# Performance work log

Measured on AMD Instinct MI355X. Metric: run time of the kernel, lower is better.

## Reference

```python
import jax, jax.numpy as jnp
import numpy as np

NLAYERS = 4
HEADS = 4
HEAD_DIM = 64
C = HEADS * HEAD_DIM  # 256
MAX_LEN = 1024


def setup_inputs() -> dict:
    key = jax.random.key(0)
    k1, k2, k3 = jax.random.split(key, 3)
    B, S = 16, 1024
    x = jax.random.normal(k1, (B, C, 1, S), dtype=jnp.float32)
    # length is only used via its static shape[0]; values are irrelevant
    length = jnp.zeros((MAX_LEN,), dtype=jnp.int32)
    # per-layer 1x1 conv weights, std=0.1 as in the torch init (squeeze the 1x1 spatial dims)
    w = jax.random.normal(k2, (NLAYERS, C, C), dtype=jnp.float32) * 0.1
    # persistent kv buffer
    kv = jax.random.normal(k3, (NLAYERS, HEADS, MAX_LEN, HEAD_DIM), dtype=jnp.float32) * 0.1
    return {"x": x, "length": length, "w": w, "kv": kv}


def reference(x, length, w, kv):
    B, _, _, S = x.shape
    L = length.shape[0]  # static slice length into kv buffer
    scale = 1.0 / jnp.sqrt(jnp.asarray(HEAD_DIM, dtype=x.dtype))
    for i in range(NLAYERS):
        # 1x1 conv == channel projection: (B,C,1,S) -> (B,C,1,S)
        x = jnp.einsum('oc,bchs->bohs', w[i], x)
        # view (B,4,64,S) then permute -> query (B,H,S,D)
        q = x.reshape(B, HEADS, HEAD_DIM, S).transpose(0, 1, 3, 2)
        kvi = kv[i, :, :L]  # (H, L, D); broadcasts over batch like the (1,H,L,D) torch slice
        # scaled dot-product attention with k == v == kvi
        scores = jnp.einsum('bhsd,hld->bhsl', q, kvi) * scale
        attn = jax.nn.softmax(scores, axis=-1)
        o = jnp.einsum('bhsl,hld->bhsd', attn, kvi)  # (B,H,S,D)
        # permute back and merge heads -> (B,256,1,S)
        x = o.transpose(0, 1, 3, 2).reshape(B, C, 1, S)
    return x
```

## Files before the change

kernel.cpp:

```cpp
#include <hip/hip_runtime.h>

#define NL   4
#define NH   4
#define HD   64
#define CD   256
#define SQL  1024
#define BB   16

typedef _Float16 half8 __attribute__((ext_vector_type(8)));
typedef _Float16 half4 __attribute__((ext_vector_type(4)));
typedef _Float16 half2v __attribute__((ext_vector_type(2)));
typedef float    f32x4 __attribute__((ext_vector_type(4)));
typedef float    f32x16 __attribute__((ext_vector_type(16)));
typedef unsigned short u16x8 __attribute__((ext_vector_type(8)));
typedef unsigned int  uint4v __attribute__((ext_vector_type(4)));

static __device__ __forceinline__ float bf2f(unsigned short u) {
    union { unsigned int i; float f; } v; v.i = ((unsigned int)u) << 16; return v.f;
}
static __device__ __forceinline__ unsigned short f2bf(float f) {
    union { float f; unsigned int i; } v; v.f = f;
    unsigned int u = v.i;
    return (unsigned short)((u + 0x7fffu + ((u >> 16) & 1u)) >> 16);
}

static __device__ __forceinline__ int detect_flag(const void* win) {
    const unsigned int* w = (const unsigned int*)win;
    int cnt = 0;
#pragma unroll 1
    for (int i = 0; i < 64; i++) {
        unsigned int lo = w[i] & 0xFFFFu;
        int e = (int)((lo >> 7) & 0xFF);
        cnt += (e >= 96 && e <= 144) ? 1 : 0;
    }
    return cnt >= 48 ? 1 : 0;
}

__global__ __launch_bounds__(256) void prep_all(const void* __restrict__ xin,
                                                const void* __restrict__ win,
                                                const void* __restrict__ kvin,
                                                _Float16* __restrict__ x16,
                                                _Float16* __restrict__ w16,
                                                _Float16* __restrict__ kaF,
                                                _Float16* __restrict__ vtF) {
    __shared__ __align__(16) _Float16 tile[64][72];
    const int bi = blockIdx.x;
    const int t = threadIdx.x;
    const int isbf = detect_flag(win);

    if (bi < 1024) {
        const int st = bi & 15, ct = (bi >> 4) & 3, b = bi >> 6;
        const int r = t >> 2, seg = t & 3;
        const size_t base = ((size_t)(b * CD + ct * 64 + r)) * SQL + st * 64 + seg * 16;
        float v[16];
        if (isbf) {
            const unsigned short* src = (const unsigned short*)xin + base;
            u16x8 u0 = *(const u16x8*)(src);
            u16x8 u1 = *(const u16x8*)(src + 8);
#pragma unroll
            for (int j = 0; j < 8; j++) { v[j] = bf2f(u0[j]); v[8 + j] = bf2f(u1[j]); }
        } else {
            const float* src = (const float*)xin + base;
#pragma unroll
            for (int c = 0; c < 4; c++) {
                f32x4 a = *(const f32x4*)(src + c * 4);
#pragma unroll
                for (int j = 0; j < 4; j++) v[c * 4 + j] = a[j];
            }
        }
#pragma unroll
        for (int j = 0; j < 16; j++) tile[r][seg * 16 + j] = (_Float16)v[j];
        __syncthreads();
        half8 o0, o1;
#pragma unroll
        for (int j = 0; j < 8; j++) { o0[j] = tile[seg * 16 + j][r]; o1[j] = tile[seg * 16 + 8 + j][r]; }
        _Float16* dt = x16 + ((size_t)(b * SQL + st * 64 + r)) * CD + ct * 64 + seg * 16;
        *(half8*)(dt) = o0;
        *(half8*)(dt + 8) = o1;
    } else if (bi < 1280) {
        const int j2 = bi - 1024;
        const int lt = j2 & 15, ih = j2 >> 4;
        const int r = t >> 2, seg = t & 3;
        const size_t base = ((size_t)(ih * SQL + lt * 64 + r)) * HD + seg * 16;
        float v[16];
        if (isbf) {
            const unsigned short* src = (const unsigned short*)kvin + base;
            u16x8 u0 = *(const u16x8*)(src);
            u16x8 u1 = *(const u16x8*)(src + 8);
#pragma unroll
            for (int j = 0; j < 8; j++) { v[j] = bf2f(u0[j]); v[8 + j] = bf2f(u1[j]); }
        } else {
            const float* src = (const float*)kvin + base;
#pragma unroll
            for (int c = 0; c < 4; c++) {
                f32x4 a = *(const f32x4*)(src + c * 4);
#pragma unroll
                for (int j = 0; j < 4; j++) v[c * 4 + j] = a[j];
            }
        }
#pragma unroll
        for (int j = 0; j < 16; j++) tile[r][seg * 16 + j] = (_Float16)v[j];
        __syncthreads();
        const int l = t & 63, hie = l >> 5, lne = l & 31;
        _Float16* kaB = kaF + ((size_t)ih << 16);
        _Float16* vtB = vtF + ((size_t)ih << 16);
#pragma unroll
        for (int it = 0; it < 2; it++) {
            const int c = (t >> 6) + it * 4;
            half8 ok = *(const half8*)(&tile[(c >> 2) * 32 + lne][(c & 3) * 16 + hie * 8]);
            half8 ov;
#pragma unroll
            for (int j = 0; j < 8; j++)
                ov[j] = tile[(c & 3) * 16 + hie * 8 + j][(c >> 2) * 32 + lne];
            *(half8*)(kaB + ((lt * 8 + c) << 9) + l * 8) = ok;
            *(half8*)(vtB + ((lt * 8 + c) << 9) + l * 8) = ov;
        }
    } else {
        const int i = (bi - 1280) * 256 + t;
        const size_t base = (size_t)i * 8;
        half8 h;
        if (isbf) {
            u16x8 u = *(const u16x8*)((const unsigned short*)win + base);
#pragma unroll
            for (int j = 0; j < 8; j++) h[j] = (_Float16)bf2f(u[j]);
        } else {
            const float* p = (const float*)win + base;
            f32x4 a0 = *(const f32x4*)(p);
            f32x4 a1 = *(const f32x4*)(p + 4);
#pragma unroll
            for (int j = 0; j < 4; j++) { h[j] = (_Float16)a0[j]; h[4 + j] = (_Float16)a1[j]; }
        }
        *(half8*)(w16 + base) = h;
    }
}

__global__ __launch_bounds__(256, 2) void layer_fused(const _Float16* __restrict__ xg,
                                                      _Float16* __restrict__ xout,
                                                      const _Float16* __restrict__ w16,
                                                      const _Float16* __restrict__ kaF,
                                                      const _Float16* __restrict__ vtF,
                                                      const void* __restrict__ win,
                                                      void* __restrict__ outp,
                                                      int L) {
    __shared__ __align__(16) _Float16 kvbuf[2][16384];
    const int sb = blockIdx.x;
    const int h  = blockIdx.y;
    const int b  = blockIdx.z;
    const int t  = threadIdx.x;
    const int wv = t >> 6, lane = t & 63, ln = lane & 31, hi = lane >> 5;
    const int s0 = sb * 128 + wv * 32;

    const _Float16* kaB = kaF + ((size_t)(L * NH + h) << 16);
    const _Float16* vtB = vtF + ((size_t)(L * NH + h) << 16);

    auto stage = [&](int lt, int buf, int hf) {
#pragma unroll
        for (int j = 0; j < 4; j++) {
            const int c = wv * 4 + j;
            const _Float16* src = (c < 8)
                ? kaB + (((lt * 8 + c) << 9))
                : vtB + (((lt * 8 + (c - 8)) << 9));
            __builtin_amdgcn_global_load_lds(
                (const __attribute__((address_space(1))) void*)(src + lane * 8),
                (__attribute__((address_space(3))) void*)(&kvbuf[buf][hf * 8192 + c * 512]),
                16, 0, 0);
        }
    };

    stage(0, 0, 0);
    stage(1, 0, 1);

    f32x16 gacc[2];
#pragma unroll
    for (int dblk = 0; dblk < 2; dblk++)
#pragma unroll
        for (int r = 0; r < 16; r++) gacc[dblk][r] = 0.0f;
    const _Float16* wb = w16 + ((size_t)L << 16) + ((size_t)(h * 64) << 8);
#pragma unroll
    for (int kc = 0; kc < 16; kc++) {
        half8 bx = *(const half8*)(xg + ((size_t)((b << 10) + s0 + ln) << 8) + kc * 16 + hi * 8);
#pragma unroll
        for (int dblk = 0; dblk < 2; dblk++) {
            half8 aw = *(const half8*)(wb + ((size_t)(dblk * 32 + ln) << 8) + kc * 16 + hi * 8);
            gacc[dblk] = __builtin_amdgcn_mfma_f32_32x32x16_f16(aw, bx, gacc[dblk], 0, 0, 0);
        }
    }

    const float sc = 0.180336880111120f;
    half8 qb[4];
#pragma unroll
    for (int dblk = 0; dblk < 2; dblk++)
#pragma unroll
        for (int k1 = 0; k1 < 2; k1++) {
            unsigned int u01 = __builtin_bit_cast(unsigned int,
                __builtin_amdgcn_cvt_pkrtz(gacc[dblk][k1 * 8 + 0] * sc, gacc[dblk][k1 * 8 + 1] * sc));
            unsigned int u23 = __builtin_bit_cast(unsigned int,
                __builtin_amdgcn_cvt_pkrtz(gacc[dblk][k1 * 8 + 2] * sc, gacc[dblk][k1 * 8 + 3] * sc));
            unsigned int w01 = __builtin_bit_cast(unsigned int,
                __builtin_amdgcn_cvt_pkrtz(gacc[dblk][k1 * 8 + 4] * sc, gacc[dblk][k1 * 8 + 5] * sc));
            unsigned int w23 = __builtin_bit_cast(unsigned int,
                __builtin_amdgcn_cvt_pkrtz(gacc[dblk][k1 * 8 + 6] * sc, gacc[dblk][k1 * 8 + 7] * sc));
            asm("v_permlane32_swap_b32 %0, %1" : "+v"(u01), "+v"(w01));
            asm("v_permlane32_swap_b32 %0, %1" : "+v"(u23), "+v"(w23));
            uint4v q; q[0] = u01; q[1] = u23; q[2] = w01; q[3] = w23;
            qb[dblk * 2 + k1] = __builtin_bit_cast(half8, q);
        }

    f32x16 oacc[2];
#pragma unroll
    for (int dblk = 0; dblk < 2; dblk++)
#pragma unroll
        for (int r = 0; r < 16; r++) oacc[dblk][r] = 0.0f;
    f32x4 rsum;
#pragma unroll
    for (int r = 0; r < 4; r++) rsum[r] = 0.0f;

    __syncthreads();

#pragma unroll 1
    for (int ltp = 0; ltp < 8; ltp++) {
        const int buf = ltp & 1;
        if (ltp < 7) { stage(2 * ltp + 2, buf ^ 1, 0); stage(2 * ltp + 3, buf ^ 1, 1); }
#pragma unroll
        for (int sub = 0; sub < 2; sub++) {
            const _Float16* base = &kvbuf[buf][sub * 8192];
            half8 kab[8];
#pragma unroll
            for (int c = 0; c < 8; c++)
                kab[c] = *(const half8*)(base + c * 512 + lane * 8);

            f32x16 stt[2];
#pragma unroll
            for (int lblk = 0; lblk < 2; lblk++)
#pragma unroll
                for (int r = 0; r < 16; r++) stt[lblk][r] = 0.0f;
            __builtin_amdgcn_s_setprio(1);
#pragma unroll
            for (int lblk = 0; lblk < 2; lblk++)
#pragma unroll
                for (int kd = 0; kd < 4; kd++)
                    stt[lblk] = __builtin_amdgcn_mfma_f32_32x32x16_f16(
                        kab[lblk * 4 + kd], qb[kd], stt[lblk], 0, 0, 0);
            __builtin_amdgcn_s_setprio(0);

            half8 vab[8];
#pragma unroll
            for (int c = 0; c < 8; c++)
                vab[c] = *(const half8*)(base + (8 + c) * 512 + lane * 8);

            half8 pb[4];
#pragma unroll
            for (int lblk = 0; lblk < 2; lblk++) {
                float e[16];
#pragma unroll
                for (int r = 0; r < 16; r++) e[r] = __builtin_amdgcn_exp2f(stt[lblk][r]);
#pragma unroll
                for (int g = 0; g < 4; g++)
                    rsum[g] += (e[g * 4 + 0] + e[g * 4 + 1]) + (e[g * 4 + 2] + e[g * 4 + 3]);
#pragma unroll
                for (int k1 = 0; k1 < 2; k1++) {
                    unsigned int u01 = __builtin_bit_cast(unsigned int,
                        __builtin_amdgcn_cvt_pkrtz(e[k1 * 8 + 0], e[k1 * 8 + 1]));
                    unsigned int u23 = __builtin_bit_cast(unsigned int,
                        __builtin_amdgcn_cvt_pkrtz(e[k1 * 8 + 2], e[k1 * 8 + 3]));
                    unsigned int w01 = __builtin_bit_cast(unsigned int,
                        __builtin_amdgcn_cvt_pkrtz(e[k1 * 8 + 4], e[k1 * 8 + 5]));
                    unsigned int w23 = __builtin_bit_cast(unsigned int,
                        __builtin_amdgcn_cvt_pkrtz(e[k1 * 8 + 6], e[k1 * 8 + 7]));
                    asm("v_permlane32_swap_b32 %0, %1" : "+v"(u01), "+v"(w01));
                    asm("v_permlane32_swap_b32 %0, %1" : "+v"(u23), "+v"(w23));
                    uint4v p; p[0] = u01; p[1] = u23; p[2] = w01; p[3] = w23;
                    pb[lblk * 2 + k1] = __builtin_bit_cast(half8, p);
                }
            }

            __builtin_amdgcn_s_setprio(1);
#pragma unroll
            for (int dblk = 0; dblk < 2; dblk++)
#pragma unroll
                for (int ks = 0; ks < 4; ks++)
                    oacc[dblk] = __builtin_amdgcn_mfma_f32_32x32x16_f16(
                        vab[dblk * 4 + ks], pb[ks], oacc[dblk], 0, 0, 0);
            __builtin_amdgcn_s_setprio(0);
        }
        __syncthreads();
    }

    float rs = (rsum[0] + rsum[1]) + (rsum[2] + rsum[3]);
    unsigned int ra = __builtin_bit_cast(unsigned int, rs);
    unsigned int rb = ra;
    asm("" : "+v"(rb));
    asm("v_permlane32_swap_b32 %0, %1" : "+v"(ra), "+v"(rb));
    const float inv = 1.0f / (__builtin_bit_cast(float, ra) + __builtin_bit_cast(float, rb));
    const int s = s0 + ln;

    if (L < NL - 1) {
#pragma unroll
        for (int dblk = 0; dblk < 2; dblk++)
#pragma unroll
            for (int q2 = 0; q2 < 4; q2++) {
                half4 hv;
#pragma unroll
                for (int r = 0; r < 4; r++) hv[r] = (_Float16)(oacc[dblk][q2 * 4 + r] * inv);
                *(half4*)(xout + (((size_t)((b << 10) + s)) << 8) +
                          (h << 6) + dblk * 32 + q2 * 8 + hi * 4) = hv;
            }
    } else if (detect_flag(win)) {
#pragma unroll
        for (int dblk = 0; dblk < 2; dblk++)
#pragma unroll
            for (int q2 = 0; q2 < 4; q2++)
#pragma unroll
                for (int r = 0; r < 4; r++) {
                    const int c = (h << 6) + dblk * 32 + q2 * 8 + hi * 4 + r;
                    ((unsigned short*)outp)[(((size_t)(b * CD + c)) << 10) + s] =
                        f2bf(oacc[dblk][q2 * 4 + r] * inv);
                }
    } else {
#pragma unroll
        for (int dblk = 0; dblk < 2; dblk++)
#pragma unroll
            for (int q2 = 0; q2 < 4; q2++)
#pragma unroll
                for (int r = 0; r < 4; r++) {
                    const int c = (h << 6) + dblk * 32 + q2 * 8 + hi * 4 + r;
                    ((float*)outp)[(((size_t)(b * CD + c)) << 10) + s] =
                        oacc[dblk][q2 * 4 + r] * inv;
                }
    }
}

extern "C" void kernel_launch(void* const* d_in, const int* in_sizes, int n_in,
                              void* d_out, int out_size, void* d_ws, size_t ws_size,
                              hipStream_t stream) {
    const void* xin = d_in[0];
    const void* win = d_in[2];
    const void* kvin = d_in[3];

    char* ws = (char*)d_ws;
    const size_t MB = 1u << 20;
    _Float16* xa  = (_Float16*)(ws);
    _Float16* xb  = (_Float16*)(ws + 8 * MB);
    _Float16* w16 = (_Float16*)(ws + 16 * MB);
    _Float16* kaF = (_Float16*)(ws + 17 * MB);
    _Float16* vtF = (_Float16*)(ws + 19 * MB);

    prep_all<<<dim3(1024 + 256 + 128), 256, 0, stream>>>(xin, win, kvin, xa, w16, kaF, vtF);

    _Float16* cur = xa;
    _Float16* nxt = xb;
    for (int i = 0; i < NL; i++) {
        layer_fused<<<dim3(SQL / 128, NH, BB), 256, 0, stream>>>(cur, nxt, w16, kaF, vtF,
                                                                 win, d_out, i);
        _Float16* tmp = cur; cur = nxt; nxt = tmp;
    }
}
```

Baseline: 204.4 us.

## Process two query sub-tiles per wave to reuse staged KV across more rows

Each wave now handles 64 query rows (two 32-row sub-tiles) instead of 32, so each K/V tile loaded into LDS and read into registers is reused for twice as many queries, and the grid is halved. Waves alternate which half of the staged KV buffer they process first, presumably to spread LDS bank traffic. The dtype detection flag is computed once in the prep kernel and passed through workspace instead of rescanning weights in the final layer. The cost is doubled accumulator register pressure, with launch bounds lowered to one block per SIMD, which cuts occupancy and latency hiding.

```diff
diff --git a/kernel.cpp b/kernel.cpp
--- a/kernel.cpp
+++ b/kernel.cpp
@@ -25,14 +25,19 @@
 }
 
 static __device__ __forceinline__ int detect_flag(const void* win) {
-    const unsigned int* w = (const unsigned int*)win;
+    const uint4v* w = (const uint4v*)win;
     int cnt = 0;
-#pragma unroll 1
-    for (int i = 0; i < 64; i++) {
-        unsigned int lo = w[i] & 0xFFFFu;
-        int e = (int)((lo >> 7) & 0xFF);
-        cnt += (e >= 96 && e <= 144) ? 1 : 0;
-    }
+    uint4v u[16];
+#pragma unroll
+    for (int i = 0; i < 16; i++) u[i] = w[i];
+#pragma unroll
+    for (int i = 0; i < 16; i++)
+#pragma unroll
+        for (int j = 0; j < 4; j++) {
+            unsigned int lo = u[i][j] & 0xFFFFu;
+            int e = (int)((lo >> 7) & 0xFF);
+            cnt += (e >= 96 && e <= 144) ? 1 : 0;
+        }
     return cnt >= 48 ? 1 : 0;
 }
 
@@ -42,7 +47,8 @@
                                                 _Float16* __restrict__ x16,
                                                 _Float16* __restrict__ w16,
                                                 _Float16* __restrict__ kaF,
-                                                _Float16* __restrict__ vtF) {
+                                                _Float16* __restrict__ vtF,
+                                                int* __restrict__ flagp) {
     __shared__ __align__(16) _Float16 tile[64][72];
     const int bi = blockIdx.x;
     const int t = threadIdx.x;
@@ -116,6 +122,7 @@
             *(half8*)(vtB + ((lt * 8 + c) << 9) + l * 8) = ov;
         }
     } else {
+        if (bi == 1280 && t == 0) *flagp = isbf;
         const int i = (bi - 1280) * 256 + t;
         const size_t base = (size_t)i * 8;
         half8 h;
@@ -134,12 +141,12 @@
     }
 }
 
-__global__ __launch_bounds__(256, 2) void layer_fused(const _Float16* __restrict__ xg,
+__global__ __launch_bounds__(256, 1) void layer_fused(const _Float16* __restrict__ xg,
                                                       _Float16* __restrict__ xout,
                                                       const _Float16* __restrict__ w16,
                                                       const _Float16* __restrict__ kaF,
                                                       const _Float16* __restrict__ vtF,
-                                                      const void* __restrict__ win,
+                                                      const int* __restrict__ flagp,
                                                       void* __restrict__ outp,
                                                       int L) {
     __shared__ __align__(16) _Float16 kvbuf[2][16384];
@@ -148,7 +155,10 @@
     const int b  = blockIdx.z;
     const int t  = threadIdx.x;
     const int wv = t >> 6, lane = t & 63, ln = lane & 31, hi = lane >> 5;
-    const int s0 = sb * 128 + wv * 32;
+    const int s0 = sb * 256 + wv * 64;
+    const int par = (sb ^ h ^ b ^ wv) & 1;
+
+    const int isbf_final = (L == NL - 1) ? *flagp : 0;
 
     const _Float16* kaB = kaF + ((size_t)(L * NH + h) << 16);
     const _Float16* vtB = vtF + ((size_t)(L * NH + h) << 16);
@@ -170,163 +180,184 @@
     stage(0, 0, 0);
     stage(1, 0, 1);
 
-    f32x16 gacc[2];
-#pragma unroll
-    for (int dblk = 0; dblk < 2; dblk++)
-#pragma unroll
-        for (int r = 0; r < 16; r++) gacc[dblk][r] = 0.0f;
+    f32x16 gacc[2][2];
+#pragma unroll
+    for (int ns = 0; ns < 2; ns++)
+#pragma unroll
+        for (int dblk = 0; dblk < 2; dblk++)
+#pragma unroll
+            for (int r = 0; r < 16; r++) gacc[ns][dblk][r] = 0.0f;
     const _Float16* wb = w16 + ((size_t)L << 16) + ((size_t)(h * 64) << 8);
 #pragma unroll
     for (int kc = 0; kc < 16; kc++) {
-        half8 bx = *(const half8*)(xg + ((size_t)((b << 10) + s0 + ln) << 8) + kc * 16 + hi * 8);
+        half8 bx0 = *(const half8*)(xg + ((size_t)((b << 10) + s0 + ln) << 8) + kc * 16 + hi * 8);
+        half8 bx1 = *(const half8*)(xg + ((size_t)((b << 10) + s0 + 32 + ln) << 8) + kc * 16 + hi * 8);
 #pragma unroll
         for (int dblk = 0; dblk < 2; dblk++) {
             half8 aw = *(const half8*)(wb + ((size_t)(dblk * 32 + ln) << 8) + kc * 16 + hi * 8);
-            gacc[dblk] = __builtin_amdgcn_mfma_f32_32x32x16_f16(aw, bx, gacc[dblk], 0, 0, 0);
+            gacc[0][dblk] = __builtin_amdgcn_mfma_f32_32x32x16_f16(aw, bx0, gacc[0][dblk], 0, 0, 0);
+            gacc[1][dblk] = __builtin_amdgcn_mfma_f32_32x32x16_f16(aw, bx1, gacc[1][dblk], 0, 0, 0);
         }
     }
 
     const float sc = 0.180336880111120f;
-    half8 qb[4];
-#pragma unroll
-    for (int dblk = 0; dblk < 2; dblk++)
-#pragma unroll
-        for (int k1 = 0; k1 < 2; k1++) {
-            unsigned int u01 = __builtin_bit_cast(unsigned int,
-                __builtin_amdgcn_cvt_pkrtz(gacc[dblk][k1 * 8 + 0] * sc, gacc[dblk][k1 * 8 + 1] * sc));
-            unsigned int u23 = __builtin_bit_cast(unsigned int,
-                __builtin_amdgcn_cvt_pkrtz(gacc[dblk][k1 * 8 + 2] * sc, gacc[dblk][k1 * 8 + 3] * sc));
-            unsigned int w01 = __builtin_bit_cast(unsigned int,
-                __builtin_amdgcn_cvt_pkrtz(gacc[dblk][k1 * 8 + 4] * sc, gacc[dblk][k1 * 8 + 5] * sc));
-            unsigned int w23 = __builtin_bit_cast(unsigned int,
-                __builtin_amdgcn_cvt_pkrtz(gacc[dblk][k1 * 8 + 6] * sc, gacc[dblk][k1 * 8 + 7] * sc));
-            asm("v_permlane32_swap_b32 %0, %1" : "+v"(u01), "+v"(w01));
-            asm("v_permlane32_swap_b32 %0, %1" : "+v"(u23), "+v"(w23));
-            uint4v q; q[0] = u01; q[1] = u23; q[2] = w01; q[3] = w23;
-            qb[dblk * 2 + k1] = __builtin_bit_cast(half8, q);
-        }
-
-    f32x16 oacc[2];
-#pragma unroll
-    for (int dblk = 0; dblk < 2; dblk++)
-#pragma unroll
-        for (int r = 0; r < 16; r++) oacc[dblk][r] = 0.0f;
-    f32x4 rsum;
-#pragma unroll
-    for (int r = 0; r < 4; r++) rsum[r] = 0.0f;
+    half8 qb[2][4];
+#pragma unroll
+    for (int ns = 0; ns < 2; ns++)
+#pragma unroll
+        for (int dblk = 0; dblk < 2; dblk++)
+#pragma unroll
+            for (int k1 = 0; k1 < 2; k1++) {
+                unsigned int u01 = __builtin_bit_cast(unsigned int,
+                    __builtin_amdgcn_cvt_pkrtz(gacc[ns][dblk][k1 * 8 + 0] * sc, gacc[ns][dblk][k1 * 8 + 1] * sc));
+                unsigned int u23 = __builtin_bit_cast(unsigned int,
+                    __builtin_amdgcn_cvt_pkrtz(gacc[ns][dblk][k1 * 8 + 2] * sc, gacc[ns][dblk][k1 * 8 + 3] * sc));
+                unsigned int w01 = __builtin_bit_cast(unsigned int,
+                    __builtin_amdgcn_cvt_pkrtz(gacc[ns][dblk][k1 * 8 + 4] * sc, gacc[ns][dblk][k1 * 8 + 5] * sc));
+                unsigned int w23 = __builtin_bit_cast(unsigned int,
+                    __builtin_amdgcn_cvt_pkrtz(gacc[ns][dblk][k1 * 8 + 6] * sc, gacc[ns][dblk][k1 * 8 + 7] * sc));
+                asm("v_permlane32_swap_b32 %0, %1" : "+v"(u01), "+v"(w01));
+                asm("v_permlane32_swap_b32 %0, %1" : "+v"(u23), "+v"(w23));
+                uint4v q; q[0] = u01; q[1] = u23; q[2] = w01; q[3] = w23;
+                qb[ns][dblk * 2 + k1] = __builtin_bit_cast(half8, q);
+            }
+
+    f32x16 oacc[2][2];
+#pragma unroll
+    for (int ns = 0; ns < 2; ns++)
+#pragma unroll
+        for (int dblk = 0; dblk < 2; dblk++)
+#pragma unroll
+            for (int r = 0; r < 16; r++) oacc[ns][dblk][r] = 0.0f;
+    f32x4 rsum[2];
+#pragma unroll
+    for (int ns = 0; ns < 2; ns++)
+#pragma unroll
+        for (int r = 0; r < 4; r++) rsum[ns][r] = 0.0f;
 
     __syncthreads();
 
 #pragma unroll 1
     for (int ltp = 0; ltp < 8; ltp++) {
         const int buf = ltp & 1;
-        if (ltp < 7) { stage(2 * ltp + 2, buf ^ 1, 0); stage(2 * ltp + 3, buf ^ 1, 1); }
-#pragma unroll
-        for (int sub = 0; sub < 2; sub++) {
-            const _Float16* base = &kvbuf[buf][sub * 8192];
+        if (ltp < 7) {
+            stage(2 * ltp + 2, buf ^ 1, 0);
+            stage(2 * ltp + 3, buf ^ 1, 1);
+        }
+
+#pragma unroll
+        for (int su = 0; su < 2; su++) {
+            const _Float16* base = &kvbuf[buf][(par ^ su) * 8192];
+
             half8 kab[8];
 #pragma unroll
-            for (int c = 0; c < 8; c++)
-                kab[c] = *(const half8*)(base + c * 512 + lane * 8);
-
-            f32x16 stt[2];
-#pragma unroll
-            for (int lblk = 0; lblk < 2; lblk++)
-#pragma unroll
-                for (int r = 0; r < 16; r++) stt[lblk][r] = 0.0f;
-            __builtin_amdgcn_s_setprio(1);
-#pragma unroll
-            for (int lblk = 0; lblk < 2; lblk++)
-#pragma unroll
-                for (int kd = 0; kd < 4; kd++)
-                    stt[lblk] = __builtin_amdgcn_mfma_f32_32x32x16_f16(
-                        kab[lblk * 4 + kd], qb[kd], stt[lblk], 0, 0, 0);
-            __builtin_amdgcn_s_setprio(0);
+            for (int c = 0; c < 8; c++) kab[c] = *(const half8*)(base + c * 512 + lane * 8);
 
             half8 vab[8];
 #pragma unroll
-            for (int c = 0; c < 8; c++)
-                vab[c] = *(const half8*)(base + (8 + c) * 512 + lane * 8);
-
-            half8 pb[4];
-#pragma unroll
-            for (int lblk = 0; lblk < 2; lblk++) {
-                float e[16];
-#pragma unroll
-                for (int r = 0; r < 16; r++) e[r] = __builtin_amdgcn_exp2f(stt[lblk][r]);
-#pragma unroll
-                for (int g = 0; g < 4; g++)
-                    rsum[g] += (e[g * 4 + 0] + e[g * 4 + 1]) + (e[g * 4 + 2] + e[g * 4 + 3]);
-#pragma unroll
-                for (int k1 = 0; k1 < 2; k1++) {
-                    unsigned int u01 = __builtin_bit_cast(unsigned int,
-                        __builtin_amdgcn_cvt_pkrtz(e[k1 * 8 + 0], e[k1 * 8 + 1]));
-                    unsigned int u23 = __builtin_bit_cast(unsigned int,
-                        __builtin_amdgcn_cvt_pkrtz(e[k1 * 8 + 2], e[k1 * 8 + 3]));
-                    unsigned int w01 = __builtin_bit_cast(unsigned int,
-                        __builtin_amdgcn_cvt_pkrtz(e[k1 * 8 + 4], e[k1 * 8 + 5]));
-                    unsigned int w23 = __builtin_bit_cast(unsigned int,
-                        __builtin_amdgcn_cvt_pkrtz(e[k1 * 8 + 6], e[k1 * 8 + 7]));
-                    asm("v_permlane32_swap_b32 %0, %1" : "+v"(u01), "+v"(w01));
-                    asm("v_permlane32_swap_b32 %0, %1" : "+v"(u23), "+v"(w23));
-                    uint4v p; p[0] = u01; p[1] = u23; p[2] = w01; p[3] = w23;
-                    pb[lblk * 2 + k1] = __builtin_bit_cast(half8, p);
+            for (int c = 0; c < 8; c++) vab[c] = *(const half8*)(base + (8 + c) * 512 + lane * 8);
+
+#pragma unroll
+            for (int ns = 0; ns < 2; ns++) {
+                f32x16 stt[2];
+#pragma unroll
+                for (int lblk = 0; lblk < 2; lblk++)
+#pragma unroll
+                    for (int r = 0; r < 16; r++) stt[lblk][r] = 0.0f;
+
+                __builtin_amdgcn_s_setprio(1);
+#pragma unroll
+                for (int lblk = 0; lblk < 2; lblk++)
+#pragma unroll
+                    for (int kd = 0; kd < 4; kd++)
+                        stt[lblk] = __builtin_amdgcn_mfma_f32_32x32x16_f16(
+                            kab[lblk * 4 + kd], qb[ns][kd], stt[lblk], 0, 0, 0);
+                __builtin_amdgcn_s_setprio(0);
+
+                half8 pb[4];
+#pragma unroll
+                for (int lblk = 0; lblk < 2; lblk++) {
+                    float e[16];
+#pragma unroll
+                    for (int r = 0; r < 16; r++) e[r] = __builtin_amdgcn_exp2f(stt[lblk][r]);
+#pragma unroll
+                    for (int g = 0; g < 4; g++)
+                        rsum[ns][g] += (e[g * 4 + 0] + e[g * 4 + 1]) + (e[g * 4 + 2] + e[g * 4 + 3]);
+#pragma unroll
+                    for (int k1 = 0; k1 < 2; k1++) {
+                        unsigned int u01 = __builtin_bit_cast(unsigned int,
+                            __builtin_amdgcn_cvt_pkrtz(e[k1 * 8 + 0], e[k1 * 8 + 1]));
+                        unsigned int u23 = __builtin_bit_cast(unsigned int,
+                            __builtin_amdgcn_cvt_pkrtz(e[k1 * 8 + 2], e[k1 * 8 + 3]));
+                        unsigned int w01 = __builtin_bit_cast(unsigned int,
+                            __builtin_amdgcn_cvt_pkrtz(e[k1 * 8 + 4], e[k1 * 8 + 5]));
+                        unsigned int w23 = __builtin_bit_cast(unsigned int,
+                            __builtin_amdgcn_cvt_pkrtz(e[k1 * 8 + 6], e[k1 * 8 + 7]));
+                        asm("v_permlane32_swap_b32 %0, %1" : "+v"(u01), "+v"(w01));
+                        asm("v_permlane32_swap_b32 %0, %1" : "+v"(u23), "+v"(w23));
+                        uint4v p; p[0] = u01; p[1] = u23; p[2] = w01; p[3] = w23;
+                        pb[lblk * 2 + k1] = __builtin_bit_cast(half8, p);
+                    }
                 }
+
+                __builtin_amdgcn_s_setprio(1);
+#pragma unroll
+                for (int dblk = 0; dblk < 2; dblk++)
+#pragma unroll
+                    for (int ks = 0; ks < 4; ks++)
+                        oacc[ns][dblk] = __builtin_amdgcn_mfma_f32_32x32x16_f16(
+                            vab[dblk * 4 + ks], pb[ks], oacc[ns][dblk], 0, 0, 0);
+                __builtin_amdgcn_s_setprio(0);
             }
-
-            __builtin_amdgcn_s_setprio(1);
+        }
+
+        __syncthreads();
+    }
+
+#pragma unroll
+    for (int ns = 0; ns < 2; ns++) {
+        float rs = (rsum[ns][0] + rsum[ns][1]) + (rsum[ns][2] + rsum[ns][3]);
+        unsigned int ra = __builtin_bit_cast(unsigned int, rs);
+        unsigned int rb = ra;
+        asm("" : "+v"(rb));
+        asm("v_permlane32_swap_b32 %0, %1" : "+v"(ra), "+v"(rb));
+        const float inv = 1.0f / (__builtin_bit_cast(float, ra) + __builtin_bit_cast(float, rb));
+        const int s = s0 + ns * 32 + ln;
+
+        if (L < NL - 1) {
 #pragma unroll
             for (int dblk = 0; dblk < 2; dblk++)
 #pragma unroll
-                for (int ks = 0; ks < 4; ks++)
-                    oacc[dblk] = __builtin_amdgcn_mfma_f32_32x32x16_f16(
-                        vab[dblk * 4 + ks], pb[ks], oacc[dblk], 0, 0, 0);
-            __builtin_amdgcn_s_setprio(0);
-        }
-        __syncthreads();
-    }
-
-    float rs = (rsum[0] + rsum[1]) + (rsum[2] + rsum[3]);
-    unsigned int ra = __builtin_bit_cast(unsigned int, rs);
-    unsigned int rb = ra;
-    asm("" : "+v"(rb));
-    asm("v_permlane32_swap_b32 %0, %1" : "+v"(ra), "+v"(rb));
-    const float inv = 1.0f / (__builtin_bit_cast(float, ra) + __builtin_bit_cast(float, rb));
-    const int s = s0 + ln;
-
-    if (L < NL - 1) {
-#pragma unroll
-        for (int dblk = 0; dblk < 2; dblk++)
-#pragma unroll
-            for (int q2 = 0; q2 < 4; q2++) {
-                half4 hv;
-#pragma unroll
-                for (int r = 0; r < 4; r++) hv[r] = (_Float16)(oacc[dblk][q2 * 4 + r] * inv);
-                *(half4*)(xout + (((size_t)((b << 10) + s)) << 8) +
-                          (h << 6) + dblk * 32 + q2 * 8 + hi * 4) = hv;
-            }
-    } else if (detect_flag(win)) {
-#pragma unroll
-        for (int dblk = 0; dblk < 2; dblk++)
-#pragma unroll
-            for (int q2 = 0; q2 < 4; q2++)
-#pragma unroll
-                for (int r = 0; r < 4; r++) {
-                    const int c = (h << 6) + dblk * 32 + q2 * 8 + hi * 4 + r;
-                    ((unsigned short*)outp)[(((size_t)(b * CD + c)) << 10) + s] =
-                        f2bf(oacc[dblk][q2 * 4 + r] * inv);
+                for (int q2 = 0; q2 < 4; q2++) {
+                    half4 hv;
+#pragma unroll
+                    for (int r = 0; r < 4; r++) hv[r] = (_Float16)(oacc[ns][dblk][q2 * 4 + r] * inv);
+                    *(half4*)(xout + (((size_t)((b << 10) + s)) << 8) +
+                              (h << 6) + dblk * 32 + q2 * 8 + hi * 4) = hv;
                 }
-    } else {
-#pragma unroll
-        for (int dblk = 0; dblk < 2; dblk++)
-#pragma unroll
-            for (int q2 = 0; q2 < 4; q2++)
-#pragma unroll
-                for (int r = 0; r < 4; r++) {
-                    const int c = (h << 6) + dblk * 32 + q2 * 8 + hi * 4 + r;
-                    ((float*)outp)[(((size_t)(b * CD + c)) << 10) + s] =
-                        oacc[dblk][q2 * 4 + r] * inv;
-                }
+        } else if (isbf_final) {
+#pragma unroll
+            for (int dblk = 0; dblk < 2; dblk++)
+#pragma unroll
+                for (int q2 = 0; q2 < 4; q2++)
+#pragma unroll
+                    for (int r = 0; r < 4; r++) {
+                        const int c = (h << 6) + dblk * 32 + q2 * 8 + hi * 4 + r;
+                        ((unsigned short*)outp)[(((size_t)(b * CD + c)) << 10) + s] =
+                            f2bf(oacc[ns][dblk][q2 * 4 + r] * inv);
+                    }
+        } else {
+#pragma unroll
+            for (int dblk = 0; dblk < 2; dblk++)
+#pragma unroll
+                for (int q2 = 0; q2 < 4; q2++)
+#pragma unroll
+                    for (int r = 0; r < 4; r++) {
+                        const int c = (h << 6) + dblk * 32 + q2 * 8 + hi * 4 + r;
+                        ((float*)outp)[(((size_t)(b * CD + c)) << 10) + s] =
+                            oacc[ns][dblk][q2 * 4 + r] * inv;
+                    }
+        }
     }
 }
 
@@ -344,14 +375,15 @@
     _Float16* w16 = (_Float16*)(ws + 16 * MB);
     _Float16* kaF = (_Float16*)(ws + 17 * MB);
     _Float16* vtF = (_Float16*)(ws + 19 * MB);
-
-    prep_all<<<dim3(1024 + 256 + 128), 256, 0, stream>>>(xin, win, kvin, xa, w16, kaF, vtF);
+    int*      flg = (int*)(ws + 21 * MB);
+
+    prep_all<<<dim3(1024 + 256 + 128), 256, 0, stream>>>(xin, win, kvin, xa, w16, kaF, vtF, flg);
 
     _Float16* cur = xa;
     _Float16* nxt = xb;
     for (int i = 0; i < NL; i++) {
-        layer_fused<<<dim3(SQL / 128, NH, BB), 256, 0, stream>>>(cur, nxt, w16, kaF, vtF,
-                                                                 win, d_out, i);
+        layer_fused<<<dim3(SQL / 256, NH, BB), 256, 0, stream>>>(cur, nxt, w16, kaF, vtF,
+                                                                 flg, d_out, i);
         _Float16* tmp = cur; cur = nxt; nxt = tmp;
     }
 }
```

Result: slower. 218.3 us (+6.8%).
